# Kernel optimization log

Measured on AMD Instinct MI355X. Metric: run time of the kernel, lower is better.

The kernel has to match this reference:

```python
import jax, jax.numpy as jnp
import numpy as np
from jax import lax

EPS = 1e-5

def layer_norm(x, g, b):
    m = x.mean(-1, keepdims=True)
    v = ((x - m) ** 2).mean(-1, keepdims=True)
    return (x - m) / jnp.sqrt(v + EPS) * g + b

def setup_inputs() -> dict:
    key = jax.random.key(0)
    ks = jax.random.split(key, 8)
    B, L, C = 8, 4096, 512
    latents = jax.random.normal(ks[0], (B, L, C), jnp.float32)
    dw_w = jax.random.normal(ks[1], (C, 1, 3), jnp.float32) * 0.02   # depthwise conv weight (O, I/g=1, K)
    dw_b = jnp.zeros((C,), jnp.float32)
    pw_w = jax.random.normal(ks[2], (C, C), jnp.float32) * 0.02      # pointwise (1x1) conv weight (out, in)
    pw_b = jnp.zeros((C,), jnp.float32)
    gate_w = jax.random.normal(ks[3], (2 * C,), jnp.float32) * 0.02  # mix_gate Linear(2C -> 1)
    gate_b = jnp.ones((), jnp.float32)                               # bias init to 1.0
    carrier_w = jax.random.normal(ks[4], (C,), jnp.float32) * 0.02   # carrier_score Linear(C -> 1)
    carrier_b = jnp.zeros((), jnp.float32)
    ln1_g = jnp.ones((C,), jnp.float32); ln1_b = jnp.zeros((C,), jnp.float32)
    ln2_g = jnp.ones((C,), jnp.float32); ln2_b = jnp.zeros((C,), jnp.float32)
    return {"latents": latents, "ln1_g": ln1_g, "ln1_b": ln1_b,
            "dw_w": dw_w, "dw_b": dw_b, "pw_w": pw_w, "pw_b": pw_b,
            "gate_w": gate_w, "gate_b": gate_b,
            "carrier_w": carrier_w, "carrier_b": carrier_b,
            "ln2_g": ln2_g, "ln2_b": ln2_b, "carrier_slots": 8}

def reference(latents, ln1_g, ln1_b, dw_w, dw_b, pw_w, pw_b,
              gate_w, gate_b, carrier_w, carrier_b, ln2_g, ln2_b, carrier_slots):
    B, L, C = latents.shape
    normalized = layer_norm(latents, ln1_g, ln1_b)          # [B, L, C]
    # depthwise conv1d: k=3, stride=2, pad=1, groups=C
    x = jnp.transpose(normalized, (0, 2, 1))                # [B, C, L]
    h = lax.conv_general_dilated(x, dw_w, window_strides=(2,), padding=[(1, 1)],
                                 feature_group_count=C,
                                 dimension_numbers=("NCH", "OIH", "NCH"))
    h = h + dw_b[None, :, None]
    h = jax.nn.gelu(h, approximate=False)                   # torch GELU default = exact erf
    reduced = jnp.einsum("oc,bcl->blo", pw_w, h) + pw_b     # pointwise 1x1 conv -> [B, Lr, C]
    # avg_pool1d(k=2, s=2, ceil_mode): L is even here so plain pairwise mean
    pooled = latents.reshape(B, L // 2, 2, C).mean(axis=2)  # [B, L/2, C]
    min_len = min(reduced.shape[1], pooled.shape[1])
    reduced = reduced[:, :min_len, :]
    pooled = pooled[:, :min_len, :]
    # gate on concat([reduced, pooled]) without materializing the concat
    logits = reduced @ gate_w[:C] + pooled @ gate_w[C:] + gate_b  # [B, min_len]
    gate = 0.5 + 0.5 * jax.nn.sigmoid(logits)[..., None]          # [B, min_len, 1]
    merged = pooled + gate * (reduced - pooled)
    if carrier_slots > 0 and L > carrier_slots:
        scores = normalized @ carrier_w + carrier_b          # [B, L]
        _, idx = lax.top_k(scores, carrier_slots)
        idx = jnp.sort(idx, axis=1)                          # [B, k]
        idx3 = jnp.broadcast_to(idx[:, :, None], (B, carrier_slots, C))
        carriers = jnp.take_along_axis(latents, idx3, axis=1)
        merged = jnp.concatenate([carriers, merged], axis=1)
    out = layer_norm(merged, ln2_g, ln2_b)                   # dropout p=0 (eval) -> identity
    return out, gate[..., 0]
```

## Files before the change

### kernel.cpp

```cpp
#include <hip/hip_runtime.h>
#include <hip/hip_bf16.h>
#include <math.h>

#define B_ 8
#define L_ 4096
#define C_ 512
#define LO_ 2048
#define SLOTS 8
#define LM_ 2056

typedef __attribute__((ext_vector_type(8))) short bf16x8;
typedef __attribute__((ext_vector_type(4))) float f32x4;
typedef unsigned short ushort_t;

__device__ __forceinline__ float waveReduceSum(float v){
  #pragma unroll
  for (int off = 32; off; off >>= 1) v += __shfl_xor(v, off);
  return v;
}

__device__ __forceinline__ unsigned short f2bf(float f){
  unsigned u = __float_as_uint(f);
  u += 0x7fffu + ((u >> 16) & 1u);
  return (unsigned short)(u >> 16);
}
__device__ __forceinline__ float bf2f(unsigned short b){
  return __uint_as_float(((unsigned)b) << 16);
}

#define GLOAD_LDS16(g, l) __builtin_amdgcn_global_load_lds( \
    (__attribute__((address_space(1))) void*)(g), \
    (__attribute__((address_space(3))) void*)(l), 16, 0, 0)

__global__ __launch_bounds__(512) void k_conv(
    const float* __restrict__ lat, const float* __restrict__ g1, const float* __restrict__ b1,
    const float* __restrict__ dw, const float* __restrict__ db,
    const float* __restrict__ cw, const float* __restrict__ cbp,
    const float* __restrict__ pw, ushort_t* __restrict__ pwb,
    ushort_t* __restrict__ hbuf, ushort_t* __restrict__ pooled, float* __restrict__ scores)
{
  __shared__ float rows[17][C_];
  __shared__ float stat[17][3];
  __shared__ float sc_[2];
  int blk = blockIdx.x;
  int b = blk >> 8;
  int chunk = blk & 255;
  int t0 = chunk * 8;
  int tid = threadIdx.x;
  int wv = tid >> 6, lane = tid & 63;
  int lbase = 16 * chunk - 1;

  if (blk < 256){
    int i = blk * 1024 + tid * 2;
    float2 v = *(const float2*)(pw + i);
    ushort2 o; o.x = f2bf(v.x); o.y = f2bf(v.y);
    *(ushort2*)(pwb + i) = o;
  }

  int c4 = lane * 4;
  float4 glo = *(const float4*)(g1 + c4);
  float4 ghi = *(const float4*)(g1 + 256 + c4);
  float4 wlo = *(const float4*)(cw + c4);
  float4 whi = *(const float4*)(cw + 256 + c4);
  float4 gclo, gchi;
  gclo.x = glo.x*wlo.x; gclo.y = glo.y*wlo.y; gclo.z = glo.z*wlo.z; gclo.w = glo.w*wlo.w;
  gchi.x = ghi.x*whi.x; gchi.y = ghi.y*whi.y; gchi.z = ghi.z*whi.z; gchi.w = ghi.w*whi.w;

  if (wv == 7){
    float4 blo = *(const float4*)(b1 + c4);
    float4 bhi = *(const float4*)(b1 + 256 + c4);
    float sgc = gclo.x+gclo.y+gclo.z+gclo.w + gchi.x+gchi.y+gchi.z+gchi.w;
    float sbc = blo.x*wlo.x + blo.y*wlo.y + blo.z*wlo.z + blo.w*wlo.w
              + bhi.x*whi.x + bhi.y*whi.y + bhi.z*whi.z + bhi.w*whi.w;
    sgc = waveReduceSum(sgc);
    sbc = waveReduceSum(sbc);
    if (lane == 0){ sc_[0] = sgc; sc_[1] = sbc; }
  }

  for (int r = wv; r < 17; r += 8){
    int l = lbase + r;
    float4 v0, v1;
    if (l >= 0){
      const float* xp = lat + ((size_t)(b * L_ + l)) * C_;
      v0 = *(const float4*)(xp + c4);
      v1 = *(const float4*)(xp + 256 + c4);
    } else {
      v0.x=0.f; v0.y=0.f; v0.z=0.f; v0.w=0.f;
      v1 = v0;
    }
    *(float4*)&rows[r][c4] = v0;
    *(float4*)&rows[r][256 + c4] = v1;
    float s1 = v0.x+v0.y+v0.z+v0.w + v1.x+v1.y+v1.z+v1.w;
    float s2 = v0.x*v0.x+v0.y*v0.y+v0.z*v0.z+v0.w*v0.w
             + v1.x*v1.x+v1.y*v1.y+v1.z*v1.z+v1.w*v1.w;
    float sd = v0.x*gclo.x+v0.y*gclo.y+v0.z*gclo.z+v0.w*gclo.w
             + v1.x*gchi.x+v1.y*gchi.y+v1.z*gchi.z+v1.w*gchi.w;
    s1 = waveReduceSum(s1);
    s2 = waveReduceSum(s2);
    sd = waveReduceSum(sd);
    if (lane == 0){
      float m = s1 * (1.f / C_);
      float var = s2 * (1.f / C_) - m * m;
      stat[r][0] = m;
      stat[r][1] = rsqrtf(var + 1e-5f);
      stat[r][2] = sd;
    }
  }
  __syncthreads();

  if (tid >= 1 && tid <= 16){
    int r = tid;
    float sc = (stat[r][2] - stat[r][0] * sc_[0]) * stat[r][1] + sc_[1] + cbp[0];
    scores[b * L_ + lbase + r] = sc;
  }

  int th = tid >> 7;
  int cq = (tid & 127) * 4;
  float4 gq = *(const float4*)(g1 + cq);
  float4 bq = *(const float4*)(b1 + cq);
  float4 dbq = *(const float4*)(db + cq);
  float4 w0 = *(const float4*)(dw + cq*3);
  float4 w1 = *(const float4*)(dw + cq*3 + 4);
  float4 w2 = *(const float4*)(dw + cq*3 + 8);
  float wk[4][3] = {{w0.x, w0.y, w0.z}, {w0.w, w1.x, w1.y},
                    {w1.z, w1.w, w2.x}, {w2.y, w2.z, w2.w}};
  float gk[4] = {gq.x, gq.y, gq.z, gq.w};
  float bk[4] = {bq.x, bq.y, bq.z, bq.w};
  float dbk[4] = {dbq.x, dbq.y, dbq.z, dbq.w};
  #pragma unroll
  for (int i = 0; i < 2; i++){
    int t = th * 2 + i;
    int rl = 2*t, rm = 2*t+1, rrg = 2*t+2;
    float4 xl = *(const float4*)&rows[rl][cq];
    float4 xm = *(const float4*)&rows[rm][cq];
    float4 xrr = *(const float4*)&rows[rrg][cq];
    float ml = stat[rl][0], rlr = stat[rl][1];
    float mm = stat[rm][0], rmr = stat[rm][1];
    float mr2 = stat[rrg][0], rrr = stat[rrg][1];
    bool zpad = (chunk == 0 && t == 0);
    float xlv[4] = {xl.x, xl.y, xl.z, xl.w};
    float xmv[4] = {xm.x, xm.y, xm.z, xm.w};
    float xrv[4] = {xrr.x, xrr.y, xrr.z, xrr.w};
    ushort4 hv, pv;
    unsigned short* hp = (unsigned short*)&hv;
    unsigned short* pp = (unsigned short*)&pv;
    #pragma unroll
    for (int k = 0; k < 4; k++){
      float n0 = zpad ? 0.f : ((xlv[k] - ml) * rlr * gk[k] + bk[k]);
      float n1 = (xmv[k] - mm) * rmr * gk[k] + bk[k];
      float n2 = (xrv[k] - mr2) * rrr * gk[k] + bk[k];
      float hh = n0 * wk[k][0] + n1 * wk[k][1] + n2 * wk[k][2] + dbk[k];
      float ge = 0.5f * hh * (1.f + erff(hh * 0.70710678118654752440f));
      hp[k] = f2bf(ge);
      pp[k] = f2bf(0.5f * (xmv[k] + xrv[k]));
    }
    size_t oidx = ((size_t)(b * LO_ + t0 + t)) * C_ + cq;
    *(ushort4*)(hbuf + oidx) = hv;
    *(ushort4*)(pooled + oidx) = pv;
  }
}

__global__ __launch_bounds__(1024) void k_topk(
    const float* __restrict__ scores, const float* __restrict__ lat,
    const float* __restrict__ g2, const float* __restrict__ b2, float* __restrict__ out)
{
  __shared__ float sv[L_];
  __shared__ float rv_[16];
  __shared__ int   ri_[16];
  __shared__ int   chosen[SLOTS];
  int b = blockIdx.x, tid = threadIdx.x;
  #pragma unroll
  for (int j = 0; j < 4; j++) sv[tid + j * 1024] = scores[b * L_ + tid + j * 1024];
  __syncthreads();
  int wv = tid >> 6, lane = tid & 63;
  for (int it = 0; it < SLOTS; it++){
    float best = -INFINITY; int bi = L_;
    #pragma unroll
    for (int j = 0; j < 4; j++){
      int i = tid + j * 1024;
      float v = sv[i];
      if (v > best || (v == best && i < bi)){ best = v; bi = i; }
    }
    #pragma unroll
    for (int off = 32; off; off >>= 1){
      float ov = __shfl_xor(best, off); int oi = __shfl_xor(bi, off);
      if (ov > best || (ov == best && oi < bi)){ best = ov; bi = oi; }
    }
    if (lane == 0){ rv_[wv] = best; ri_[wv] = bi; }
    __syncthreads();
    if (tid == 0){
      for (int w2 = 1; w2 < 16; w2++){
        if (rv_[w2] > best || (rv_[w2] == best && ri_[w2] < bi)){ best = rv_[w2]; bi = ri_[w2]; }
      }
      chosen[it] = bi;
      sv[bi] = -INFINITY;
    }
    __syncthreads();
  }
  if (tid == 0){
    for (int i = 0; i < SLOTS; i++)
      for (int j = i + 1; j < SLOTS; j++)
        if (chosen[j] < chosen[i]){ int t = chosen[i]; chosen[i] = chosen[j]; chosen[j] = t; }
  }
  __syncthreads();
  if (wv < SLOTS){
    int s = wv;
    int l = chosen[s];
    const float* x = lat + ((size_t)(b * L_ + l)) * C_;
    float xs[8];
    float s1 = 0.f, s2 = 0.f;
    #pragma unroll
    for (int i = 0; i < 2; i++){
      float4 vv = *(const float4*)(x + i * 256 + lane * 4);
      xs[i*4+0] = vv.x; xs[i*4+1] = vv.y; xs[i*4+2] = vv.z; xs[i*4+3] = vv.w;
      s1 += vv.x + vv.y + vv.z + vv.w;
      s2 += vv.x*vv.x + vv.y*vv.y + vv.z*vv.z + vv.w*vv.w;
    }
    s1 = waveReduceSum(s1); s2 = waveReduceSum(s2);
    float m = s1 * (1.f / C_);
    float rstd = rsqrtf(s2 * (1.f / C_) - m * m + 1e-5f);
    float* o = out + ((size_t)(b * LM_ + s)) * C_;
    #pragma unroll
    for (int i = 0; i < 2; i++){
      int cc = i * 256 + lane * 4;
      float4 gv = *(const float4*)(g2 + cc);
      float4 bv = *(const float4*)(b2 + cc);
      float4 ov;
      ov.x = (xs[i*4+0] - m) * rstd * gv.x + bv.x;
      ov.y = (xs[i*4+1] - m) * rstd * gv.y + bv.y;
      ov.z = (xs[i*4+2] - m) * rstd * gv.z + bv.z;
      ov.w = (xs[i*4+3] - m) * rstd * gv.w + bv.w;
      *(float4*)(o + cc) = ov;
    }
  }
}

__global__ __launch_bounds__(256) void k_gemm(
    const ushort_t* __restrict__ A, const ushort_t* __restrict__ Bw,
    const float* __restrict__ bias, ushort_t* __restrict__ Cout)
{
  __shared__ short As[2][128][32];
  __shared__ short Bs[2][128][32];
  int tid = threadIdx.x;
  int w = tid >> 6, lane = tid & 63;
  int hw = blockIdx.y * 4 + blockIdx.x;
  int tile = ((hw & 7) << 6) | (hw >> 3);
  int row0 = (tile >> 2) * 128, col0 = (tile & 3) * 128;
  int wr = (w >> 1) * 64, wc = (w & 1) * 64;
  int srow = lane >> 2;
  int scol = (lane & 3) * 8;
  int fr = lane & 15, kq = (lane >> 4) * 8;

  f32x4 acc[4][4];
  #pragma unroll
  for (int m = 0; m < 4; m++)
    #pragma unroll
    for (int n = 0; n < 4; n++)
      acc[m][n] = (f32x4){0.f, 0.f, 0.f, 0.f};

  #pragma unroll
  for (int j = 0; j < 2; j++){
    int i = 2*w + j;
    GLOAD_LDS16(A  + (size_t)(row0 + 16*i + srow) * C_ + scol, &As[0][16*i][0]);
    GLOAD_LDS16(Bw + (size_t)(col0 + 16*i + srow) * C_ + scol, &Bs[0][16*i][0]);
  }
  __syncthreads();

  int cur = 0;
  for (int kt = 0; kt < 16; kt++){
    if (kt < 15){
      int k0n = (kt + 1) * 32;
      #pragma unroll
      for (int j = 0; j < 2; j++){
        int i = 2*w + j;
        GLOAD_LDS16(A  + (size_t)(row0 + 16*i + srow) * C_ + k0n + scol, &As[cur^1][16*i][0]);
        GLOAD_LDS16(Bw + (size_t)(col0 + 16*i + srow) * C_ + k0n + scol, &Bs[cur^1][16*i][0]);
      }
    }
    bf16x8 af[4], bfr[4];
    #pragma unroll
    for (int m = 0; m < 4; m++) af[m]  = *(const bf16x8*)&As[cur][wr + m*16 + fr][kq];
    #pragma unroll
    for (int n = 0; n < 4; n++) bfr[n] = *(const bf16x8*)&Bs[cur][wc + n*16 + fr][kq];
    #pragma unroll
    for (int m = 0; m < 4; m++)
      #pragma unroll
      for (int n = 0; n < 4; n++)
        acc[m][n] = __builtin_amdgcn_mfma_f32_16x16x32_bf16(af[m], bfr[n], acc[m][n], 0, 0, 0);
    __syncthreads();
    cur ^= 1;
  }

  int cq = lane & 15, rq = (lane >> 4) * 4;
  #pragma unroll
  for (int n = 0; n < 4; n++){
    int col = col0 + wc + n*16 + cq;
    float bv = bias[col];
    #pragma unroll
    for (int m = 0; m < 4; m++){
      #pragma unroll
      for (int j = 0; j < 4; j++){
        int row = row0 + wr + m*16 + rq + j;
        Cout[(size_t)row * C_ + col] = f2bf(acc[m][n][j] + bv);
      }
    }
  }
}

__global__ __launch_bounds__(256) void k_epilogue(
    const ushort_t* __restrict__ red, const ushort_t* __restrict__ pooled,
    const float* __restrict__ gw, const float* __restrict__ gbp,
    const float* __restrict__ g2, const float* __restrict__ b2,
    float* __restrict__ out, float* __restrict__ gateout)
{
  int row  = blockIdx.x * 4 + (threadIdx.x >> 6);
  int lane = threadIdx.x & 63;
  int b = row >> 11, l = row & (LO_ - 1);
  const ushort_t* rr = red + (size_t)row * C_;
  const ushort_t* pp = pooled + (size_t)row * C_;
  float rv[8], pv[8];
  float lp = 0.f;
  #pragma unroll
  for (int i = 0; i < 2; i++){
    int c = i * 256 + lane * 4;
    ushort4 r4 = *(const ushort4*)(rr + c);
    ushort4 p4 = *(const ushort4*)(pp + c);
    float4 w1 = *(const float4*)(gw + c);
    float4 w2 = *(const float4*)(gw + C_ + c);
    float r0 = bf2f(r4.x), r1 = bf2f(r4.y), r2 = bf2f(r4.z), r3 = bf2f(r4.w);
    float q0 = bf2f(p4.x), q1 = bf2f(p4.y), q2 = bf2f(p4.z), q3 = bf2f(p4.w);
    rv[i*4+0] = r0; rv[i*4+1] = r1; rv[i*4+2] = r2; rv[i*4+3] = r3;
    pv[i*4+0] = q0; pv[i*4+1] = q1; pv[i*4+2] = q2; pv[i*4+3] = q3;
    lp += r0*w1.x + r1*w1.y + r2*w1.z + r3*w1.w
        + q0*w2.x + q1*w2.y + q2*w2.z + q3*w2.w;
  }
  lp = waveReduceSum(lp);
  float gate = 0.5f + 0.5f / (1.f + expf(-(lp + gbp[0])));
  float mv[8];
  float s1 = 0.f, s2 = 0.f;
  #pragma unroll
  for (int j = 0; j < 8; j++){
    mv[j] = pv[j] + gate * (rv[j] - pv[j]);
    s1 += mv[j]; s2 += mv[j] * mv[j];
  }
  s1 = waveReduceSum(s1); s2 = waveReduceSum(s2);
  float m = s1 * (1.f / C_);
  float rstd = rsqrtf(s2 * (1.f / C_) - m * m + 1e-5f);
  float* o = out + ((size_t)(b * LM_ + SLOTS + l)) * C_;
  #pragma unroll
  for (int i = 0; i < 2; i++){
    int c = i * 256 + lane * 4;
    float4 gv = *(const float4*)(g2 + c);
    float4 bv = *(const float4*)(b2 + c);
    float4 ov;
    ov.x = (mv[i*4+0] - m) * rstd * gv.x + bv.x;
    ov.y = (mv[i*4+1] - m) * rstd * gv.y + bv.y;
    ov.z = (mv[i*4+2] - m) * rstd * gv.z + bv.z;
    ov.w = (mv[i*4+3] - m) * rstd * gv.w + bv.w;
    *(float4*)(o + c) = ov;
  }
  if (lane == 0) gateout[b * LO_ + l] = gate;
}

extern "C" void kernel_launch(void* const* d_in, const int* in_sizes, int n_in,
                              void* d_out, int out_size, void* d_ws, size_t ws_size,
                              hipStream_t stream)
{
  const float* lat = (const float*)d_in[0];
  const float* g1  = (const float*)d_in[1];
  const float* b1  = (const float*)d_in[2];
  const float* dw  = (const float*)d_in[3];
  const float* db  = (const float*)d_in[4];
  const float* pw  = (const float*)d_in[5];
  const float* pb  = (const float*)d_in[6];
  const float* gw  = (const float*)d_in[7];
  const float* gb  = (const float*)d_in[8];
  const float* cw  = (const float*)d_in[9];
  const float* cb  = (const float*)d_in[10];
  const float* g2  = (const float*)d_in[11];
  const float* b2  = (const float*)d_in[12];

  float* out = (float*)d_out;
  float* gateout = out + (size_t)B_ * LM_ * C_;

  const size_t NHL = (size_t)B_ * LO_ * C_;
  ushort_t* hbuf   = (ushort_t*)d_ws;
  ushort_t* pooled = hbuf + NHL;
  ushort_t* redb   = pooled + NHL;
  ushort_t* pwb    = redb + NHL;
  float*    scores = (float*)(pwb + (size_t)C_ * C_);

  hipLaunchKernelGGL(k_conv,    dim3(B_ * LO_ / 8), dim3(512), 0, stream,
                     lat, g1, b1, dw, db, cw, cb, pw, pwb, hbuf, pooled, scores);
  hipLaunchKernelGGL(k_topk,    dim3(B_), dim3(1024), 0, stream, scores, lat, g2, b2, out);
  hipLaunchKernelGGL(k_gemm,    dim3(4, 128), dim3(256), 0, stream, hbuf, pwb, pb, redb);
  hipLaunchKernelGGL(k_epilogue,dim3(B_ * LO_ / 4), dim3(256), 0, stream, redb, pooled, gw, gb, g2, b2, out, gateout);
}
```

Before: 75.96 us.

## Fuse conv, pointwise GEMM and gated LayerNorm epilogue into one kernel

The LayerNorm+depthwise conv+GELU stage, the bf16 MFMA pointwise GEMM and the gate/merge/LayerNorm epilogue are merged into a single kernel. Each block handles 64 output rows and keeps the GELU activations as a swizzled LDS A tile. It streams the bf16 weight matrix through double-buffered LDS, then stages the GEMM result in a reused LDS buffer for the epilogue. This removes the global round-trips for the h, pooled and reduced intermediates and two launches. In exchange, every block re-reads the full weight matrix from L2 and uses about 132KB of LDS, so only one 512-thread block fits per CU. The pooled values and gate logits stay in fp32, and the weight cast moves into a separate small kernel.

Measured after the change: 131.1 us. 72.5% more time.

```diff
diff --git a/kernel.cpp b/kernel.cpp
--- a/kernel.cpp
+++ b/kernel.cpp
@@ -18,145 +18,255 @@
   for (int off = 32; off; off >>= 1) v += __shfl_xor(v, off);
   return v;
 }
-
 __device__ __forceinline__ unsigned short f2bf(float f){
   unsigned u = __float_as_uint(f);
   u += 0x7fffu + ((u >> 16) & 1u);
   return (unsigned short)(u >> 16);
 }
-__device__ __forceinline__ float bf2f(unsigned short b){
-  return __uint_as_float(((unsigned)b) << 16);
-}
+__device__ __forceinline__ float dot4(float4 a, float4 b){
+  return a.x*b.x + a.y*b.y + a.z*b.z + a.w*b.w;
+}
+__device__ __forceinline__ float sum4(float4 a){ return a.x + a.y + a.z + a.w; }
 
 #define GLOAD_LDS16(g, l) __builtin_amdgcn_global_load_lds( \
     (__attribute__((address_space(1))) void*)(g), \
     (__attribute__((address_space(3))) void*)(l), 16, 0, 0)
 
-__global__ __launch_bounds__(512) void k_conv(
-    const float* __restrict__ lat, const float* __restrict__ g1, const float* __restrict__ b1,
+__global__ __launch_bounds__(256) void k_cast(const float* __restrict__ src, ushort_t* __restrict__ dst){
+  int i = (blockIdx.x * 256 + threadIdx.x) * 4;
+  float4 v = *(const float4*)(src + i);
+  ushort4 o;
+  o.x = f2bf(v.x); o.y = f2bf(v.y); o.z = f2bf(v.z); o.w = f2bf(v.w);
+  *(ushort4*)(dst + i) = o;
+}
+
+__global__ __launch_bounds__(512, 2) void k_mega(
+    const float* __restrict__ lat,
+    const float* __restrict__ g1, const float* __restrict__ b1,
     const float* __restrict__ dw, const float* __restrict__ db,
     const float* __restrict__ cw, const float* __restrict__ cbp,
-    const float* __restrict__ pw, ushort_t* __restrict__ pwb,
-    ushort_t* __restrict__ hbuf, ushort_t* __restrict__ pooled, float* __restrict__ scores)
+    const float* __restrict__ gw, const float* __restrict__ gbp,
+    const float* __restrict__ pb, const ushort_t* __restrict__ pwb,
+    const float* __restrict__ g2, const float* __restrict__ b2,
+    float* __restrict__ scores, float* __restrict__ out, float* __restrict__ gateout)
 {
-  __shared__ float rows[17][C_];
-  __shared__ float stat[17][3];
-  __shared__ float sc_[2];
+  __shared__ union UU {
+    struct { ushort_t A[64*512]; ushort_t Bs[2][512*32]; } p;
+    float red[64*516];
+  } u;
+  __shared__ float plog[64];
+
   int blk = blockIdx.x;
-  int b = blk >> 8;
-  int chunk = blk & 255;
-  int t0 = chunk * 8;
+  int b = blk >> 5, chunk = blk & 31;
+  int t0 = chunk * 64;
   int tid = threadIdx.x;
-  int wv = tid >> 6, lane = tid & 63;
-  int lbase = 16 * chunk - 1;
-
-  if (blk < 256){
-    int i = blk * 1024 + tid * 2;
-    float2 v = *(const float2*)(pw + i);
-    ushort2 o; o.x = f2bf(v.x); o.y = f2bf(v.y);
-    *(ushort2*)(pwb + i) = o;
-  }
-
+  int w = tid >> 6, lane = tid & 63;
   int c4 = lane * 4;
-  float4 glo = *(const float4*)(g1 + c4);
-  float4 ghi = *(const float4*)(g1 + 256 + c4);
-  float4 wlo = *(const float4*)(cw + c4);
-  float4 whi = *(const float4*)(cw + 256 + c4);
+
+  float4 g1lo = *(const float4*)(g1 + c4);
+  float4 g1hi = *(const float4*)(g1 + 256 + c4);
+  float4 b1lo = *(const float4*)(b1 + c4);
+  float4 b1hi = *(const float4*)(b1 + 256 + c4);
+  float4 cwlo = *(const float4*)(cw + c4);
+  float4 cwhi = *(const float4*)(cw + 256 + c4);
   float4 gclo, gchi;
-  gclo.x = glo.x*wlo.x; gclo.y = glo.y*wlo.y; gclo.z = glo.z*wlo.z; gclo.w = glo.w*wlo.w;
-  gchi.x = ghi.x*whi.x; gchi.y = ghi.y*whi.y; gchi.z = ghi.z*whi.z; gchi.w = ghi.w*whi.w;
-
-  if (wv == 7){
-    float4 blo = *(const float4*)(b1 + c4);
-    float4 bhi = *(const float4*)(b1 + 256 + c4);
-    float sgc = gclo.x+gclo.y+gclo.z+gclo.w + gchi.x+gchi.y+gchi.z+gchi.w;
-    float sbc = blo.x*wlo.x + blo.y*wlo.y + blo.z*wlo.z + blo.w*wlo.w
-              + bhi.x*whi.x + bhi.y*whi.y + bhi.z*whi.z + bhi.w*whi.w;
-    sgc = waveReduceSum(sgc);
-    sbc = waveReduceSum(sbc);
-    if (lane == 0){ sc_[0] = sgc; sc_[1] = sbc; }
-  }
-
-  for (int r = wv; r < 17; r += 8){
-    int l = lbase + r;
-    float4 v0, v1;
-    if (l >= 0){
-      const float* xp = lat + ((size_t)(b * L_ + l)) * C_;
-      v0 = *(const float4*)(xp + c4);
-      v1 = *(const float4*)(xp + 256 + c4);
-    } else {
-      v0.x=0.f; v0.y=0.f; v0.z=0.f; v0.w=0.f;
-      v1 = v0;
-    }
-    *(float4*)&rows[r][c4] = v0;
-    *(float4*)&rows[r][256 + c4] = v1;
-    float s1 = v0.x+v0.y+v0.z+v0.w + v1.x+v1.y+v1.z+v1.w;
-    float s2 = v0.x*v0.x+v0.y*v0.y+v0.z*v0.z+v0.w*v0.w
-             + v1.x*v1.x+v1.y*v1.y+v1.z*v1.z+v1.w*v1.w;
-    float sd = v0.x*gclo.x+v0.y*gclo.y+v0.z*gclo.z+v0.w*gclo.w
-             + v1.x*gchi.x+v1.y*gchi.y+v1.z*gchi.z+v1.w*gchi.w;
-    s1 = waveReduceSum(s1);
-    s2 = waveReduceSum(s2);
-    sd = waveReduceSum(sd);
-    if (lane == 0){
-      float m = s1 * (1.f / C_);
-      float var = s2 * (1.f / C_) - m * m;
-      stat[r][0] = m;
-      stat[r][1] = rsqrtf(var + 1e-5f);
-      stat[r][2] = sd;
-    }
-  }
-  __syncthreads();
-
-  if (tid >= 1 && tid <= 16){
-    int r = tid;
-    float sc = (stat[r][2] - stat[r][0] * sc_[0]) * stat[r][1] + sc_[1] + cbp[0];
-    scores[b * L_ + lbase + r] = sc;
-  }
-
-  int th = tid >> 7;
-  int cq = (tid & 127) * 4;
-  float4 gq = *(const float4*)(g1 + cq);
-  float4 bq = *(const float4*)(b1 + cq);
-  float4 dbq = *(const float4*)(db + cq);
-  float4 w0 = *(const float4*)(dw + cq*3);
-  float4 w1 = *(const float4*)(dw + cq*3 + 4);
-  float4 w2 = *(const float4*)(dw + cq*3 + 8);
-  float wk[4][3] = {{w0.x, w0.y, w0.z}, {w0.w, w1.x, w1.y},
-                    {w1.z, w1.w, w2.x}, {w2.y, w2.z, w2.w}};
-  float gk[4] = {gq.x, gq.y, gq.z, gq.w};
-  float bk[4] = {bq.x, bq.y, bq.z, bq.w};
-  float dbk[4] = {dbq.x, dbq.y, dbq.z, dbq.w};
-  #pragma unroll
-  for (int i = 0; i < 2; i++){
-    int t = th * 2 + i;
-    int rl = 2*t, rm = 2*t+1, rrg = 2*t+2;
-    float4 xl = *(const float4*)&rows[rl][cq];
-    float4 xm = *(const float4*)&rows[rm][cq];
-    float4 xrr = *(const float4*)&rows[rrg][cq];
-    float ml = stat[rl][0], rlr = stat[rl][1];
-    float mm = stat[rm][0], rmr = stat[rm][1];
-    float mr2 = stat[rrg][0], rrr = stat[rrg][1];
-    bool zpad = (chunk == 0 && t == 0);
-    float xlv[4] = {xl.x, xl.y, xl.z, xl.w};
-    float xmv[4] = {xm.x, xm.y, xm.z, xm.w};
-    float xrv[4] = {xrr.x, xrr.y, xrr.z, xrr.w};
-    ushort4 hv, pv;
-    unsigned short* hp = (unsigned short*)&hv;
-    unsigned short* pp = (unsigned short*)&pv;
-    #pragma unroll
-    for (int k = 0; k < 4; k++){
-      float n0 = zpad ? 0.f : ((xlv[k] - ml) * rlr * gk[k] + bk[k]);
-      float n1 = (xmv[k] - mm) * rmr * gk[k] + bk[k];
-      float n2 = (xrv[k] - mr2) * rrr * gk[k] + bk[k];
-      float hh = n0 * wk[k][0] + n1 * wk[k][1] + n2 * wk[k][2] + dbk[k];
-      float ge = 0.5f * hh * (1.f + erff(hh * 0.70710678118654752440f));
-      hp[k] = f2bf(ge);
-      pp[k] = f2bf(0.5f * (xmv[k] + xrv[k]));
-    }
-    size_t oidx = ((size_t)(b * LO_ + t0 + t)) * C_ + cq;
-    *(ushort4*)(hbuf + oidx) = hv;
-    *(ushort4*)(pooled + oidx) = pv;
+  gclo.x = g1lo.x*cwlo.x; gclo.y = g1lo.y*cwlo.y; gclo.z = g1lo.z*cwlo.z; gclo.w = g1lo.w*cwlo.w;
+  gchi.x = g1hi.x*cwhi.x; gchi.y = g1hi.y*cwhi.y; gchi.z = g1hi.z*cwhi.z; gchi.w = g1hi.w*cwhi.w;
+  float sgc = waveReduceSum(sum4(gclo) + sum4(gchi));
+  float sbc = waveReduceSum(dot4(b1lo, cwlo) + dot4(b1hi, cwhi));
+  float cb0 = cbp[0];
+  float4 dwl0 = *(const float4*)(dw + c4*3);
+  float4 dwl1 = *(const float4*)(dw + c4*3 + 4);
+  float4 dwl2 = *(const float4*)(dw + c4*3 + 8);
+  float4 dwh0 = *(const float4*)(dw + c4*3 + 768);
+  float4 dwh1 = *(const float4*)(dw + c4*3 + 772);
+  float4 dwh2 = *(const float4*)(dw + c4*3 + 776);
+  float4 dblo = *(const float4*)(db + c4);
+  float4 dbhi = *(const float4*)(db + 256 + c4);
+  float4 gw2lo = *(const float4*)(gw + C_ + c4);
+  float4 gw2hi = *(const float4*)(gw + C_ + 256 + c4);
+
+  float4 plo[8], phi[8];
+
+  #pragma unroll
+  for (int j = 0; j < 2; j++){
+    int lbase = 2*t0 + 16*w + 8*j - 1;
+    float4 xlo[9], xhi[9];
+    float m9[9], rs9[9];
+    #pragma unroll
+    for (int r = 0; r < 9; r++){
+      int gl = lbase + r;
+      if (gl >= 0){
+        const float* xp = lat + ((size_t)(b * L_ + gl)) * C_;
+        xlo[r] = *(const float4*)(xp + c4);
+        xhi[r] = *(const float4*)(xp + 256 + c4);
+      } else {
+        xlo[r].x = 0.f; xlo[r].y = 0.f; xlo[r].z = 0.f; xlo[r].w = 0.f;
+        xhi[r] = xlo[r];
+      }
+      float s1 = sum4(xlo[r]) + sum4(xhi[r]);
+      float s2 = dot4(xlo[r], xlo[r]) + dot4(xhi[r], xhi[r]);
+      float sd = dot4(xlo[r], gclo) + dot4(xhi[r], gchi);
+      s1 = waveReduceSum(s1); s2 = waveReduceSum(s2); sd = waveReduceSum(sd);
+      float mm = s1 * (1.f / C_);
+      float var = s2 * (1.f / C_) - mm * mm;
+      float rstd = rsqrtf(var + 1e-5f);
+      m9[r] = mm; rs9[r] = rstd;
+      if (r >= 1 && lane == r - 1){
+        scores[b * L_ + gl] = (sd - mm * sgc) * rstd + sbc + cb0;
+      }
+    }
+    float wtl[4][3] = {{dwl0.x,dwl0.y,dwl0.z},{dwl0.w,dwl1.x,dwl1.y},
+                       {dwl1.z,dwl1.w,dwl2.x},{dwl2.y,dwl2.z,dwl2.w}};
+    float wth[4][3] = {{dwh0.x,dwh0.y,dwh0.z},{dwh0.w,dwh1.x,dwh1.y},
+                       {dwh1.z,dwh1.w,dwh2.x},{dwh2.y,dwh2.z,dwh2.w}};
+    #pragma unroll
+    for (int i2 = 0; i2 < 4; i2++){
+      int arow = w*8 + 4*j + i2;
+      int rA = 2*i2, rB2 = 2*i2+1, rC2 = 2*i2+2;
+      bool zpad = (chunk == 0 && arow == 0);
+      float mA = m9[rA], rsA = rs9[rA];
+      float mB = m9[rB2], rsB = rs9[rB2];
+      float mC = m9[rC2], rsC = rs9[rC2];
+      ushort4 hv, hv2;
+      float4 pl, ph;
+#define CONV1(xa,xb,xc,gg,bb,w0t,w1t,w2t,dbv,OUTH,OUTP) { \
+      float n0 = zpad ? 0.f : (((xa) - mA) * rsA * (gg) + (bb)); \
+      float n1 = ((xb) - mB) * rsB * (gg) + (bb); \
+      float n2 = ((xc) - mC) * rsC * (gg) + (bb); \
+      float hh = n0*(w0t) + n1*(w1t) + n2*(w2t) + (dbv); \
+      OUTH = f2bf(0.5f*hh*(1.f + erff(hh*0.70710678118654752440f))); \
+      OUTP = 0.5f*((xb) + (xc)); }
+      CONV1(xlo[rA].x, xlo[rB2].x, xlo[rC2].x, g1lo.x, b1lo.x, wtl[0][0],wtl[0][1],wtl[0][2], dblo.x, hv.x, pl.x);
+      CONV1(xlo[rA].y, xlo[rB2].y, xlo[rC2].y, g1lo.y, b1lo.y, wtl[1][0],wtl[1][1],wtl[1][2], dblo.y, hv.y, pl.y);
+      CONV1(xlo[rA].z, xlo[rB2].z, xlo[rC2].z, g1lo.z, b1lo.z, wtl[2][0],wtl[2][1],wtl[2][2], dblo.z, hv.z, pl.z);
+      CONV1(xlo[rA].w, xlo[rB2].w, xlo[rC2].w, g1lo.w, b1lo.w, wtl[3][0],wtl[3][1],wtl[3][2], dblo.w, hv.w, pl.w);
+      CONV1(xhi[rA].x, xhi[rB2].x, xhi[rC2].x, g1hi.x, b1hi.x, wth[0][0],wth[0][1],wth[0][2], dbhi.x, hv2.x, ph.x);
+      CONV1(xhi[rA].y, xhi[rB2].y, xhi[rC2].y, g1hi.y, b1hi.y, wth[1][0],wth[1][1],wth[1][2], dbhi.y, hv2.y, ph.y);
+      CONV1(xhi[rA].z, xhi[rB2].z, xhi[rC2].z, g1hi.z, b1hi.z, wth[2][0],wth[2][1],wth[2][2], dbhi.z, hv2.z, ph.z);
+      CONV1(xhi[rA].w, xhi[rB2].w, xhi[rC2].w, g1hi.w, b1hi.w, wth[3][0],wth[3][1],wth[3][2], dbhi.w, hv2.w, ph.w);
+#undef CONV1
+      plo[4*j + i2] = pl;
+      phi[4*j + i2] = ph;
+      int swz = (arow & 7) * 8;
+      *(ushort4*)&u.p.A[(size_t)arow*512 + (c4 ^ swz)]         = hv;
+      *(ushort4*)&u.p.A[(size_t)arow*512 + ((c4 ^ swz) + 256)] = hv2;
+    }
+  }
+  #pragma unroll
+  for (int i = 0; i < 8; i++){
+    float pp = dot4(plo[i], gw2lo) + dot4(phi[i], gw2hi);
+    pp = waveReduceSum(pp);
+    if (lane == 0) plog[w*8 + i] = pp;
+  }
+  __syncthreads();
+
+  int fr = lane & 15, kq = (lane >> 4) * 8;
+  int wc = w * 64;
+  f32x4 acc[4][4];
+  #pragma unroll
+  for (int m = 0; m < 4; m++)
+    #pragma unroll
+    for (int n = 0; n < 4; n++)
+      acc[m][n] = (f32x4){0.f, 0.f, 0.f, 0.f};
+
+  int sIdx0 = tid * 8;
+  #pragma unroll
+  for (int rr = 0; rr < 4; rr++){
+    int sIdx = rr * 4096 + sIdx0;
+    int orow = sIdx >> 5;
+    int coff = sIdx & 31;
+    GLOAD_LDS16(pwb + (size_t)orow * C_ + coff, &u.p.Bs[0][sIdx]);
+  }
+  __syncthreads();
+
+  for (int kt = 0; kt < 16; kt++){
+    int cur = kt & 1;
+    if (kt < 15){
+      int k0n = (kt + 1) * 32;
+      #pragma unroll
+      for (int rr = 0; rr < 4; rr++){
+        int sIdx = rr * 4096 + sIdx0;
+        int orow = sIdx >> 5;
+        int coff = sIdx & 31;
+        GLOAD_LDS16(pwb + (size_t)orow * C_ + k0n + coff, &u.p.Bs[cur^1][sIdx]);
+      }
+    }
+    bf16x8 af[4], bfr[4];
+    #pragma unroll
+    for (int m = 0; m < 4; m++){
+      int ar = m*16 + fr;
+      af[m] = *(const bf16x8*)&u.p.A[(size_t)ar*512 + ((kt*32 + kq) ^ ((ar & 7) * 8))];
+    }
+    #pragma unroll
+    for (int n = 0; n < 4; n++)
+      bfr[n] = *(const bf16x8*)&u.p.Bs[cur][(wc + n*16 + fr)*32 + kq];
+    #pragma unroll
+    for (int m = 0; m < 4; m++)
+      #pragma unroll
+      for (int n = 0; n < 4; n++)
+        acc[m][n] = __builtin_amdgcn_mfma_f32_16x16x32_bf16(af[m], bfr[n], acc[m][n], 0, 0, 0);
+    __syncthreads();
+  }
+
+  {
+    int cq = fr, rq = (lane >> 4) * 4;
+    #pragma unroll
+    for (int n = 0; n < 4; n++){
+      int col = wc + n*16 + cq;
+      float pbv = pb[col];
+      #pragma unroll
+      for (int m = 0; m < 4; m++)
+        #pragma unroll
+        for (int jj = 0; jj < 4; jj++)
+          u.red[(size_t)(m*16 + rq + jj) * 516 + col] = acc[m][n][jj] + pbv;
+    }
+  }
+  __syncthreads();
+
+  float4 gw1lo = *(const float4*)(gw + c4);
+  float4 gw1hi = *(const float4*)(gw + 256 + c4);
+  float4 g2lo = *(const float4*)(g2 + c4);
+  float4 g2hi = *(const float4*)(g2 + 256 + c4);
+  float4 b2lo = *(const float4*)(b2 + c4);
+  float4 b2hi = *(const float4*)(b2 + 256 + c4);
+  float gb0 = gbp[0];
+  #pragma unroll
+  for (int i = 0; i < 8; i++){
+    int r = w*8 + i;
+    float4 rlo = *(const float4*)&u.red[(size_t)r*516 + c4];
+    float4 rhi = *(const float4*)&u.red[(size_t)r*516 + 256 + c4];
+    float rdot = dot4(rlo, gw1lo) + dot4(rhi, gw1hi);
+    rdot = waveReduceSum(rdot);
+    float logit = rdot + plog[r] + gb0;
+    float gate = 0.5f + 0.5f / (1.f + expf(-logit));
+    float4 mlo, mhi;
+    mlo.x = plo[i].x + gate * (rlo.x - plo[i].x);
+    mlo.y = plo[i].y + gate * (rlo.y - plo[i].y);
+    mlo.z = plo[i].z + gate * (rlo.z - plo[i].z);
+    mlo.w = plo[i].w + gate * (rlo.w - plo[i].w);
+    mhi.x = phi[i].x + gate * (rhi.x - phi[i].x);
+    mhi.y = phi[i].y + gate * (rhi.y - phi[i].y);
+    mhi.z = phi[i].z + gate * (rhi.z - phi[i].z);
+    mhi.w = phi[i].w + gate * (rhi.w - phi[i].w);
+    float s1 = sum4(mlo) + sum4(mhi);
+    float s2 = dot4(mlo, mlo) + dot4(mhi, mhi);
+    s1 = waveReduceSum(s1); s2 = waveReduceSum(s2);
+    float mean = s1 * (1.f / C_);
+    float rstd = rsqrtf(s2 * (1.f / C_) - mean * mean + 1e-5f);
+    float* op = out + ((size_t)(b * LM_ + SLOTS + t0 + r)) * C_;
+    float4 olo, ohi;
+    olo.x = (mlo.x - mean) * rstd * g2lo.x + b2lo.x;
+    olo.y = (mlo.y - mean) * rstd * g2lo.y + b2lo.y;
+    olo.z = (mlo.z - mean) * rstd * g2lo.z + b2lo.z;
+    olo.w = (mlo.w - mean) * rstd * g2lo.w + b2lo.w;
+    ohi.x = (mhi.x - mean) * rstd * g2hi.x + b2hi.x;
+    ohi.y = (mhi.y - mean) * rstd * g2hi.y + b2hi.y;
+    ohi.z = (mhi.z - mean) * rstd * g2hi.z + b2hi.z;
+    ohi.w = (mhi.w - mean) * rstd * g2hi.w + b2hi.w;
+    *(float4*)(op + c4) = olo;
+    *(float4*)(op + 256 + c4) = ohi;
+    if (lane == 0) gateout[b * LO_ + t0 + r] = gate;
   }
 }
 
@@ -233,133 +343,6 @@
       *(float4*)(o + cc) = ov;
     }
   }
-}
-
-__global__ __launch_bounds__(256) void k_gemm(
-    const ushort_t* __restrict__ A, const ushort_t* __restrict__ Bw,
-    const float* __restrict__ bias, ushort_t* __restrict__ Cout)
-{
-  __shared__ short As[2][128][32];
-  __shared__ short Bs[2][128][32];
-  int tid = threadIdx.x;
-  int w = tid >> 6, lane = tid & 63;
-  int hw = blockIdx.y * 4 + blockIdx.x;
-  int tile = ((hw & 7) << 6) | (hw >> 3);
-  int row0 = (tile >> 2) * 128, col0 = (tile & 3) * 128;
-  int wr = (w >> 1) * 64, wc = (w & 1) * 64;
-  int srow = lane >> 2;
-  int scol = (lane & 3) * 8;
-  int fr = lane & 15, kq = (lane >> 4) * 8;
-
-  f32x4 acc[4][4];
-  #pragma unroll
-  for (int m = 0; m < 4; m++)
-    #pragma unroll
-    for (int n = 0; n < 4; n++)
-      acc[m][n] = (f32x4){0.f, 0.f, 0.f, 0.f};
-
-  #pragma unroll
-  for (int j = 0; j < 2; j++){
-    int i = 2*w + j;
-    GLOAD_LDS16(A  + (size_t)(row0 + 16*i + srow) * C_ + scol, &As[0][16*i][0]);
-    GLOAD_LDS16(Bw + (size_t)(col0 + 16*i + srow) * C_ + scol, &Bs[0][16*i][0]);
-  }
-  __syncthreads();
-
-  int cur = 0;
-  for (int kt = 0; kt < 16; kt++){
-    if (kt < 15){
-      int k0n = (kt + 1) * 32;
-      #pragma unroll
-      for (int j = 0; j < 2; j++){
-        int i = 2*w + j;
-        GLOAD_LDS16(A  + (size_t)(row0 + 16*i + srow) * C_ + k0n + scol, &As[cur^1][16*i][0]);
-        GLOAD_LDS16(Bw + (size_t)(col0 + 16*i + srow) * C_ + k0n + scol, &Bs[cur^1][16*i][0]);
-      }
-    }
-    bf16x8 af[4], bfr[4];
-    #pragma unroll
-    for (int m = 0; m < 4; m++) af[m]  = *(const bf16x8*)&As[cur][wr + m*16 + fr][kq];
-    #pragma unroll
-    for (int n = 0; n < 4; n++) bfr[n] = *(const bf16x8*)&Bs[cur][wc + n*16 + fr][kq];
-    #pragma unroll
-    for (int m = 0; m < 4; m++)
-      #pragma unroll
-      for (int n = 0; n < 4; n++)
-        acc[m][n] = __builtin_amdgcn_mfma_f32_16x16x32_bf16(af[m], bfr[n], acc[m][n], 0, 0, 0);
-    __syncthreads();
-    cur ^= 1;
-  }
-
-  int cq = lane & 15, rq = (lane >> 4) * 4;
-  #pragma unroll
-  for (int n = 0; n < 4; n++){
-    int col = col0 + wc + n*16 + cq;
-    float bv = bias[col];
-    #pragma unroll
-    for (int m = 0; m < 4; m++){
-      #pragma unroll
-      for (int j = 0; j < 4; j++){
-        int row = row0 + wr + m*16 + rq + j;
-        Cout[(size_t)row * C_ + col] = f2bf(acc[m][n][j] + bv);
-      }
-    }
-  }
-}
-
-__global__ __launch_bounds__(256) void k_epilogue(
-    const ushort_t* __restrict__ red, const ushort_t* __restrict__ pooled,
-    const float* __restrict__ gw, const float* __restrict__ gbp,
-    const float* __restrict__ g2, const float* __restrict__ b2,
-    float* __restrict__ out, float* __restrict__ gateout)
-{
-  int row  = blockIdx.x * 4 + (threadIdx.x >> 6);
-  int lane = threadIdx.x & 63;
-  int b = row >> 11, l = row & (LO_ - 1);
-  const ushort_t* rr = red + (size_t)row * C_;
-  const ushort_t* pp = pooled + (size_t)row * C_;
-  float rv[8], pv[8];
-  float lp = 0.f;
-  #pragma unroll
-  for (int i = 0; i < 2; i++){
-    int c = i * 256 + lane * 4;
-    ushort4 r4 = *(const ushort4*)(rr + c);
-    ushort4 p4 = *(const ushort4*)(pp + c);
-    float4 w1 = *(const float4*)(gw + c);
-    float4 w2 = *(const float4*)(gw + C_ + c);
-    float r0 = bf2f(r4.x), r1 = bf2f(r4.y), r2 = bf2f(r4.z), r3 = bf2f(r4.w);
-    float q0 = bf2f(p4.x), q1 = bf2f(p4.y), q2 = bf2f(p4.z), q3 = bf2f(p4.w);
-    rv[i*4+0] = r0; rv[i*4+1] = r1; rv[i*4+2] = r2; rv[i*4+3] = r3;
-    pv[i*4+0] = q0; pv[i*4+1] = q1; pv[i*4+2] = q2; pv[i*4+3] = q3;
-    lp += r0*w1.x + r1*w1.y + r2*w1.z + r3*w1.w
-        + q0*w2.x + q1*w2.y + q2*w2.z + q3*w2.w;
-  }
-  lp = waveReduceSum(lp);
-  float gate = 0.5f + 0.5f / (1.f + expf(-(lp + gbp[0])));
-  float mv[8];
-  float s1 = 0.f, s2 = 0.f;
-  #pragma unroll
-  for (int j = 0; j < 8; j++){
-    mv[j] = pv[j] + gate * (rv[j] - pv[j]);
-    s1 += mv[j]; s2 += mv[j] * mv[j];
-  }
-  s1 = waveReduceSum(s1); s2 = waveReduceSum(s2);
-  float m = s1 * (1.f / C_);
-  float rstd = rsqrtf(s2 * (1.f / C_) - m * m + 1e-5f);
-  float* o = out + ((size_t)(b * LM_ + SLOTS + l)) * C_;
-  #pragma unroll
-  for (int i = 0; i < 2; i++){
-    int c = i * 256 + lane * 4;
-    float4 gv = *(const float4*)(g2 + c);
-    float4 bv = *(const float4*)(b2 + c);
-    float4 ov;
-    ov.x = (mv[i*4+0] - m) * rstd * gv.x + bv.x;
-    ov.y = (mv[i*4+1] - m) * rstd * gv.y + bv.y;
-    ov.z = (mv[i*4+2] - m) * rstd * gv.z + bv.z;
-    ov.w = (mv[i*4+3] - m) * rstd * gv.w + bv.w;
-    *(float4*)(o + c) = ov;
-  }
-  if (lane == 0) gateout[b * LO_ + l] = gate;
 }
 
 extern "C" void kernel_launch(void* const* d_in, const int* in_sizes, int n_in,
@@ -383,16 +366,12 @@
   float* out = (float*)d_out;
   float* gateout = out + (size_t)B_ * LM_ * C_;
 
-  const size_t NHL = (size_t)B_ * LO_ * C_;
-  ushort_t* hbuf   = (ushort_t*)d_ws;
-  ushort_t* pooled = hbuf + NHL;
-  ushort_t* redb   = pooled + NHL;
-  ushort_t* pwb    = redb + NHL;
+  ushort_t* pwb    = (ushort_t*)d_ws;
   float*    scores = (float*)(pwb + (size_t)C_ * C_);
 
-  hipLaunchKernelGGL(k_conv,    dim3(B_ * LO_ / 8), dim3(512), 0, stream,
-                     lat, g1, b1, dw, db, cw, cb, pw, pwb, hbuf, pooled, scores);
-  hipLaunchKernelGGL(k_topk,    dim3(B_), dim3(1024), 0, stream, scores, lat, g2, b2, out);
-  hipLaunchKernelGGL(k_gemm,    dim3(4, 128), dim3(256), 0, stream, hbuf, pwb, pb, redb);
-  hipLaunchKernelGGL(k_epilogue,dim3(B_ * LO_ / 4), dim3(256), 0, stream, redb, pooled, gw, gb, g2, b2, out, gateout);
-}
+  hipLaunchKernelGGL(k_cast, dim3(C_ * C_ / 1024), dim3(256), 0, stream, pw, pwb);
+  hipLaunchKernelGGL(k_mega, dim3(B_ * 32), dim3(512), 0, stream,
+                     lat, g1, b1, dw, db, cw, cb, gw, gb, pb, pwb, g2, b2,
+                     scores, out, gateout);
+  hipLaunchKernelGGL(k_topk, dim3(B_), dim3(1024), 0, stream, scores, lat, g2, b2, out);
+}
```

## Fuse pointwise GEMM with gate and LayerNorm epilogue using full-row tiles

Applied to the files above, without the earlier changes.

Replaces the separate GEMM and epilogue kernels with one kernel. Each block computes a 64-row by 512-column output tile, so full rows are available for the gate dot product and the second LayerNorm. The reduced activations are staged through shared memory instead of being written to and re-read from a bf16 global buffer, which removes that round trip and one launch. In exchange, every block reloads the whole 512x512 weight matrix, there are only 256 blocks, and the large LDS footprint may limit occupancy.

Result: slower. 102.6 us (+35.1%).

```diff
diff --git a/kernel.cpp b/kernel.cpp
--- a/kernel.cpp
+++ b/kernel.cpp
@@ -18,7 +18,6 @@
   for (int off = 32; off; off >>= 1) v += __shfl_xor(v, off);
   return v;
 }
-
 __device__ __forceinline__ unsigned short f2bf(float f){
   unsigned u = __float_as_uint(f);
   u += 0x7fffu + ((u >> 16) & 1u);
@@ -27,6 +26,10 @@
 __device__ __forceinline__ float bf2f(unsigned short b){
   return __uint_as_float(((unsigned)b) << 16);
 }
+__device__ __forceinline__ float dot4(float4 a, float4 b){
+  return a.x*b.x + a.y*b.y + a.z*b.z + a.w*b.w;
+}
+__device__ __forceinline__ float sum4(float4 a){ return a.x + a.y + a.z + a.w; }
 
 #define GLOAD_LDS16(g, l) __builtin_amdgcn_global_load_lds( \
     (__attribute__((address_space(1))) void*)(g), \
@@ -69,11 +72,8 @@
   if (wv == 7){
     float4 blo = *(const float4*)(b1 + c4);
     float4 bhi = *(const float4*)(b1 + 256 + c4);
-    float sgc = gclo.x+gclo.y+gclo.z+gclo.w + gchi.x+gchi.y+gchi.z+gchi.w;
-    float sbc = blo.x*wlo.x + blo.y*wlo.y + blo.z*wlo.z + blo.w*wlo.w
-              + bhi.x*whi.x + bhi.y*whi.y + bhi.z*whi.z + bhi.w*whi.w;
-    sgc = waveReduceSum(sgc);
-    sbc = waveReduceSum(sbc);
+    float sgc = waveReduceSum(sum4(gclo) + sum4(gchi));
+    float sbc = waveReduceSum(dot4(blo, wlo) + dot4(bhi, whi));
     if (lane == 0){ sc_[0] = sgc; sc_[1] = sbc; }
   }
 
@@ -90,14 +90,9 @@
     }
     *(float4*)&rows[r][c4] = v0;
     *(float4*)&rows[r][256 + c4] = v1;
-    float s1 = v0.x+v0.y+v0.z+v0.w + v1.x+v1.y+v1.z+v1.w;
-    float s2 = v0.x*v0.x+v0.y*v0.y+v0.z*v0.z+v0.w*v0.w
-             + v1.x*v1.x+v1.y*v1.y+v1.z*v1.z+v1.w*v1.w;
-    float sd = v0.x*gclo.x+v0.y*gclo.y+v0.z*gclo.z+v0.w*gclo.w
-             + v1.x*gchi.x+v1.y*gchi.y+v1.z*gchi.z+v1.w*gchi.w;
-    s1 = waveReduceSum(s1);
-    s2 = waveReduceSum(s2);
-    sd = waveReduceSum(sd);
+    float s1 = waveReduceSum(sum4(v0) + sum4(v1));
+    float s2 = waveReduceSum(dot4(v0, v0) + dot4(v1, v1));
+    float sd = waveReduceSum(dot4(v0, gclo) + dot4(v1, gchi));
     if (lane == 0){
       float m = s1 * (1.f / C_);
       float var = s2 * (1.f / C_) - m * m;
@@ -160,6 +155,145 @@
   }
 }
 
+__global__ __launch_bounds__(512, 4) void k_gemmepi(
+    const ushort_t* __restrict__ Ah, const ushort_t* __restrict__ Bw,
+    const float* __restrict__ pb, const ushort_t* __restrict__ pooled,
+    const float* __restrict__ gw, const float* __restrict__ gbp,
+    const float* __restrict__ g2, const float* __restrict__ b2,
+    float* __restrict__ out, float* __restrict__ gateout)
+{
+  __shared__ union UU {
+    struct { ushort_t As[2][64*32]; ushort_t Bs[2][512*32]; } g;
+    float red[16*516];
+  } u;
+
+  int blk = blockIdx.x;
+  int R0 = blk * 64;
+  int tid = threadIdx.x;
+  int w = tid >> 6, lane = tid & 63;
+  const ushort_t* Ap = Ah + (size_t)R0 * C_;
+
+#define STAGE(buf, kt) { \
+    int kk = (kt) * 32; \
+    if (w < 4){ \
+      int ar = w*16 + (lane>>2); \
+      GLOAD_LDS16(Ap + (size_t)ar*C_ + kk + (lane&3)*8, &u.g.As[buf][w*16*32]); \
+    } \
+    _Pragma("unroll") \
+    for (int uu = 0; uu < 4; uu++){ \
+      int unit = w + uu*8; \
+      int brow = unit*16 + (lane>>2); \
+      GLOAD_LDS16(Bw + (size_t)brow*C_ + kk + (lane&3)*8, &u.g.Bs[buf][unit*16*32]); \
+    } }
+
+  int fr = lane & 15, kq = (lane >> 4) * 8;
+  int wc = w * 64;
+  f32x4 acc[4][4];
+  #pragma unroll
+  for (int m = 0; m < 4; m++)
+    #pragma unroll
+    for (int n = 0; n < 4; n++)
+      acc[m][n] = (f32x4){0.f, 0.f, 0.f, 0.f};
+
+  STAGE(0, 0);
+  __syncthreads();
+  for (int kt = 0; kt < 16; kt++){
+    int cur = kt & 1;
+    if (kt < 15){ STAGE(cur ^ 1, kt + 1); }
+    bf16x8 af[4], bfr[4];
+    #pragma unroll
+    for (int m = 0; m < 4; m++)
+      af[m] = *(const bf16x8*)&u.g.As[cur][(m*16 + fr)*32 + kq];
+    #pragma unroll
+    for (int n = 0; n < 4; n++)
+      bfr[n] = *(const bf16x8*)&u.g.Bs[cur][(wc + n*16 + fr)*32 + kq];
+    #pragma unroll
+    for (int m = 0; m < 4; m++)
+      #pragma unroll
+      for (int n = 0; n < 4; n++)
+        acc[m][n] = __builtin_amdgcn_mfma_f32_16x16x32_bf16(af[m], bfr[n], acc[m][n], 0, 0, 0);
+    __syncthreads();
+  }
+#undef STAGE
+
+  int cq = fr, rq = (lane >> 4) * 4;
+  #pragma unroll
+  for (int n = 0; n < 4; n++){
+    float pbv = pb[wc + n*16 + cq];
+    #pragma unroll
+    for (int m = 0; m < 4; m++)
+      #pragma unroll
+      for (int j = 0; j < 4; j++)
+        acc[m][n][j] += pbv;
+  }
+
+  int c4 = lane * 4;
+  float4 gw1lo = *(const float4*)(gw + c4);
+  float4 gw1hi = *(const float4*)(gw + 256 + c4);
+  float4 gw2lo = *(const float4*)(gw + C_ + c4);
+  float4 gw2hi = *(const float4*)(gw + C_ + 256 + c4);
+  float4 g2lo = *(const float4*)(g2 + c4);
+  float4 g2hi = *(const float4*)(g2 + 256 + c4);
+  float4 b2lo = *(const float4*)(b2 + c4);
+  float4 b2hi = *(const float4*)(b2 + 256 + c4);
+  float gb0 = gbp[0];
+
+  #pragma unroll
+  for (int g = 0; g < 4; g++){
+    #pragma unroll
+    for (int n = 0; n < 4; n++)
+      #pragma unroll
+      for (int j = 0; j < 4; j++)
+        u.red[(rq + j)*516 + wc + n*16 + cq] = acc[g][n][j];
+    __syncthreads();
+    #pragma unroll
+    for (int rr = 0; rr < 2; rr++){
+      int rloc = w*2 + rr;
+      int grow = R0 + g*16 + rloc;
+      const float* redrow = &u.red[rloc * 516];
+      float4 rlo = *(const float4*)&redrow[c4];
+      float4 rhi = *(const float4*)&redrow[256 + c4];
+      const ushort_t* prow = pooled + (size_t)grow * C_;
+      ushort4 p4l = *(const ushort4*)(prow + c4);
+      ushort4 p4h = *(const ushort4*)(prow + 256 + c4);
+      float4 plov, phiv;
+      plov.x = bf2f(p4l.x); plov.y = bf2f(p4l.y); plov.z = bf2f(p4l.z); plov.w = bf2f(p4l.w);
+      phiv.x = bf2f(p4h.x); phiv.y = bf2f(p4h.y); phiv.z = bf2f(p4h.z); phiv.w = bf2f(p4h.w);
+      float rdot = waveReduceSum(dot4(rlo, gw1lo) + dot4(rhi, gw1hi));
+      float pdot = waveReduceSum(dot4(plov, gw2lo) + dot4(phiv, gw2hi));
+      float gate = 0.5f + 0.5f / (1.f + expf(-(rdot + pdot + gb0)));
+      float4 mlo, mhi;
+      mlo.x = plov.x + gate * (rlo.x - plov.x);
+      mlo.y = plov.y + gate * (rlo.y - plov.y);
+      mlo.z = plov.z + gate * (rlo.z - plov.z);
+      mlo.w = plov.w + gate * (rlo.w - plov.w);
+      mhi.x = phiv.x + gate * (rhi.x - phiv.x);
+      mhi.y = phiv.y + gate * (rhi.y - phiv.y);
+      mhi.z = phiv.z + gate * (rhi.z - phiv.z);
+      mhi.w = phiv.w + gate * (rhi.w - phiv.w);
+      float s1 = waveReduceSum(sum4(mlo) + sum4(mhi));
+      float s2 = waveReduceSum(dot4(mlo, mlo) + dot4(mhi, mhi));
+      float mean = s1 * (1.f / C_);
+      float rstd = rsqrtf(s2 * (1.f / C_) - mean * mean + 1e-5f);
+      int b = grow >> 11, l = grow & (LO_ - 1);
+      float* op = out + ((size_t)(b * LM_ + SLOTS + l)) * C_;
+      float4 olo, ohi;
+      olo.x = (mlo.x - mean) * rstd * g2lo.x + b2lo.x;
+      olo.y = (mlo.y - mean) * rstd * g2lo.y + b2lo.y;
+      olo.z = (mlo.z - mean) * rstd * g2lo.z + b2lo.z;
+      olo.w = (mlo.w - mean) * rstd * g2lo.w + b2lo.w;
+      ohi.x = (mhi.x - mean) * rstd * g2hi.x + b2hi.x;
+      ohi.y = (mhi.y - mean) * rstd * g2hi.y + b2hi.y;
+      ohi.z = (mhi.z - mean) * rstd * g2hi.z + b2hi.z;
+      ohi.w = (mhi.w - mean) * rstd * g2hi.w + b2hi.w;
+      *(float4*)(op + c4) = olo;
+      *(float4*)(op + 256 + c4) = ohi;
+      if (lane == 0) gateout[grow] = gate;
+    }
+    __syncthreads();
+  }
+}
+
 __global__ __launch_bounds__(1024) void k_topk(
     const float* __restrict__ scores, const float* __restrict__ lat,
     const float* __restrict__ g2, const float* __restrict__ b2, float* __restrict__ out)
@@ -233,133 +367,6 @@
       *(float4*)(o + cc) = ov;
     }
   }
-}
-
-__global__ __launch_bounds__(256) void k_gemm(
-    const ushort_t* __restrict__ A, const ushort_t* __restrict__ Bw,
-    const float* __restrict__ bias, ushort_t* __restrict__ Cout)
-{
-  __shared__ short As[2][128][32];
-  __shared__ short Bs[2][128][32];
-  int tid = threadIdx.x;
-  int w = tid >> 6, lane = tid & 63;
-  int hw = blockIdx.y * 4 + blockIdx.x;
-  int tile = ((hw & 7) << 6) | (hw >> 3);
-  int row0 = (tile >> 2) * 128, col0 = (tile & 3) * 128;
-  int wr = (w >> 1) * 64, wc = (w & 1) * 64;
-  int srow = lane >> 2;
-  int scol = (lane & 3) * 8;
-  int fr = lane & 15, kq = (lane >> 4) * 8;
-
-  f32x4 acc[4][4];
-  #pragma unroll
-  for (int m = 0; m < 4; m++)
-    #pragma unroll
-    for (int n = 0; n < 4; n++)
-      acc[m][n] = (f32x4){0.f, 0.f, 0.f, 0.f};
-
-  #pragma unroll
-  for (int j = 0; j < 2; j++){
-    int i = 2*w + j;
-    GLOAD_LDS16(A  + (size_t)(row0 + 16*i + srow) * C_ + scol, &As[0][16*i][0]);
-    GLOAD_LDS16(Bw + (size_t)(col0 + 16*i + srow) * C_ + scol, &Bs[0][16*i][0]);
-  }
-  __syncthreads();
-
-  int cur = 0;
-  for (int kt = 0; kt < 16; kt++){
-    if (kt < 15){
-      int k0n = (kt + 1) * 32;
-      #pragma unroll
-      for (int j = 0; j < 2; j++){
-        int i = 2*w + j;
-        GLOAD_LDS16(A  + (size_t)(row0 + 16*i + srow) * C_ + k0n + scol, &As[cur^1][16*i][0]);
-        GLOAD_LDS16(Bw + (size_t)(col0 + 16*i + srow) * C_ + k0n + scol, &Bs[cur^1][16*i][0]);
-      }
-    }
-    bf16x8 af[4], bfr[4];
-    #pragma unroll
-    for (int m = 0; m < 4; m++) af[m]  = *(const bf16x8*)&As[cur][wr + m*16 + fr][kq];
-    #pragma unroll
-    for (int n = 0; n < 4; n++) bfr[n] = *(const bf16x8*)&Bs[cur][wc + n*16 + fr][kq];
-    #pragma unroll
-    for (int m = 0; m < 4; m++)
-      #pragma unroll
-      for (int n = 0; n < 4; n++)
-        acc[m][n] = __builtin_amdgcn_mfma_f32_16x16x32_bf16(af[m], bfr[n], acc[m][n], 0, 0, 0);
-    __syncthreads();
-    cur ^= 1;
-  }
-
-  int cq = lane & 15, rq = (lane >> 4) * 4;
-  #pragma unroll
-  for (int n = 0; n < 4; n++){
-    int col = col0 + wc + n*16 + cq;
-    float bv = bias[col];
-    #pragma unroll
-    for (int m = 0; m < 4; m++){
-      #pragma unroll
-      for (int j = 0; j < 4; j++){
-        int row = row0 + wr + m*16 + rq + j;
-        Cout[(size_t)row * C_ + col] = f2bf(acc[m][n][j] + bv);
-      }
-    }
-  }
-}
-
-__global__ __launch_bounds__(256) void k_epilogue(
-    const ushort_t* __restrict__ red, const ushort_t* __restrict__ pooled,
-    const float* __restrict__ gw, const float* __restrict__ gbp,
-    const float* __restrict__ g2, const float* __restrict__ b2,
-    float* __restrict__ out, float* __restrict__ gateout)
-{
-  int row  = blockIdx.x * 4 + (threadIdx.x >> 6);
-  int lane = threadIdx.x & 63;
-  int b = row >> 11, l = row & (LO_ - 1);
-  const ushort_t* rr = red + (size_t)row * C_;
-  const ushort_t* pp = pooled + (size_t)row * C_;
-  float rv[8], pv[8];
-  float lp = 0.f;
-  #pragma unroll
-  for (int i = 0; i < 2; i++){
-    int c = i * 256 + lane * 4;
-    ushort4 r4 = *(const ushort4*)(rr + c);
-    ushort4 p4 = *(const ushort4*)(pp + c);
-    float4 w1 = *(const float4*)(gw + c);
-    float4 w2 = *(const float4*)(gw + C_ + c);
-    float r0 = bf2f(r4.x), r1 = bf2f(r4.y), r2 = bf2f(r4.z), r3 = bf2f(r4.w);
-    float q0 = bf2f(p4.x), q1 = bf2f(p4.y), q2 = bf2f(p4.z), q3 = bf2f(p4.w);
-    rv[i*4+0] = r0; rv[i*4+1] = r1; rv[i*4+2] = r2; rv[i*4+3] = r3;
-    pv[i*4+0] = q0; pv[i*4+1] = q1; pv[i*4+2] = q2; pv[i*4+3] = q3;
-    lp += r0*w1.x + r1*w1.y + r2*w1.z + r3*w1.w
-        + q0*w2.x + q1*w2.y + q2*w2.z + q3*w2.w;
-  }
-  lp = waveReduceSum(lp);
-  float gate = 0.5f + 0.5f / (1.f + expf(-(lp + gbp[0])));
-  float mv[8];
-  float s1 = 0.f, s2 = 0.f;
-  #pragma unroll
-  for (int j = 0; j < 8; j++){
-    mv[j] = pv[j] + gate * (rv[j] - pv[j]);
-    s1 += mv[j]; s2 += mv[j] * mv[j];
-  }
-  s1 = waveReduceSum(s1); s2 = waveReduceSum(s2);
-  float m = s1 * (1.f / C_);
-  float rstd = rsqrtf(s2 * (1.f / C_) - m * m + 1e-5f);
-  float* o = out + ((size_t)(b * LM_ + SLOTS + l)) * C_;
-  #pragma unroll
-  for (int i = 0; i < 2; i++){
-    int c = i * 256 + lane * 4;
-    float4 gv = *(const float4*)(g2 + c);
-    float4 bv = *(const float4*)(b2 + c);
-    float4 ov;
-    ov.x = (mv[i*4+0] - m) * rstd * gv.x + bv.x;
-    ov.y = (mv[i*4+1] - m) * rstd * gv.y + bv.y;
-    ov.z = (mv[i*4+2] - m) * rstd * gv.z + bv.z;
-    ov.w = (mv[i*4+3] - m) * rstd * gv.w + bv.w;
-    *(float4*)(o + c) = ov;
-  }
-  if (lane == 0) gateout[b * LO_ + l] = gate;
 }
 
 extern "C" void kernel_launch(void* const* d_in, const int* in_sizes, int n_in,
@@ -386,13 +393,12 @@
   const size_t NHL = (size_t)B_ * LO_ * C_;
   ushort_t* hbuf   = (ushort_t*)d_ws;
   ushort_t* pooled = hbuf + NHL;
-  ushort_t* redb   = pooled + NHL;
-  ushort_t* pwb    = redb + NHL;
+  ushort_t* pwb    = pooled + NHL;
   float*    scores = (float*)(pwb + (size_t)C_ * C_);
 
   hipLaunchKernelGGL(k_conv,    dim3(B_ * LO_ / 8), dim3(512), 0, stream,
                      lat, g1, b1, dw, db, cw, cb, pw, pwb, hbuf, pooled, scores);
+  hipLaunchKernelGGL(k_gemmepi, dim3(B_ * LO_ / 64), dim3(512), 0, stream,
+                     hbuf, pwb, pb, pooled, gw, gb, g2, b2, out, gateout);
   hipLaunchKernelGGL(k_topk,    dim3(B_), dim3(1024), 0, stream, scores, lat, g2, b2, out);
-  hipLaunchKernelGGL(k_gemm,    dim3(4, 128), dim3(256), 0, stream, hbuf, pwb, pb, redb);
-  hipLaunchKernelGGL(k_epilogue,dim3(B_ * LO_ / 4), dim3(256), 0, stream, redb, pooled, gw, gb, g2, b2, out, gateout);
-}
+}
```
